# Performance work log

Hardware: AMD Instinct MI355X
Metric: run time of the kernel (lower is better)

Reference implementation:

```python
import jax, jax.numpy as jnp
import numpy as np

N_ATOMS, N_EDGES, FEAT, N_RBF, N_CONV = 20000, 320000, 128, 20, 3
CUTOFF = 5.0
ATOM_FEA, H_FEA, N_OUT, VOCAB = 64, 128, 5, 100


def _dense(x, W, b):
    return x @ W + b


def _painn_forward(xyz, embed, W1, b1, W2, b2, Wd, bd, U, V, Ws1, bs1, Ws2, bs2,
                   Wr1, br1, Wr2, br2, Wf1, bf1, Wf2, bf2, Wf3, bf3, z, nbrs):
    act = jax.nn.silu
    i_idx, j_idx = nbrs[:, 0], nbrs[:, 1]          # receiver i, sender j
    r_ij = xyz[j_idx] - xyz[i_idx]                 # [E,3]
    d = jnp.sqrt(jnp.sum(r_ij ** 2, -1) + 1e-12)   # [E]
    unit = r_ij / d[:, None]
    n = jnp.arange(1, N_RBF + 1, dtype=xyz.dtype)
    rbf = jnp.sin(n[None, :] * jnp.pi * d[:, None] / CUTOFF) / d[:, None]   # [E,n_rbf]
    f_cut = 0.5 * (jnp.cos(jnp.pi * d / CUTOFF) + 1.0) * (d < CUTOFF)       # cosine envelope

    s = embed[z]                                   # [N,F]
    v = jnp.zeros((s.shape[0], FEAT, 3), s.dtype)  # [N,F,3]

    for l in range(N_CONV):
        # ---- message block ----
        phi = _dense(act(_dense(s, W1[l], b1[l])), W2[l], b2[l])        # [N,3F]
        w_s = _dense(rbf, Wd[l], bd[l]) * f_cut[:, None]                # [E,3F]
        inv = (phi[j_idx] * w_s).reshape(-1, 3, FEAT)                   # [E,3,F]
        dv_ij = unit[:, None, :] * inv[:, 2, :, None] + inv[:, 0, :, None] * v[j_idx]  # [E,F,3]
        s = s + jax.ops.segment_sum(inv[:, 1, :], i_idx, num_segments=N_ATOMS)
        v = v + jax.ops.segment_sum(dv_ij, i_idx, num_segments=N_ATOMS)
        # ---- update block ----
        u_v = jnp.einsum('nfd,fg->ngd', v, U[l])                        # [N,F,3]
        v_v = jnp.einsum('nfd,fg->ngd', v, V[l])
        v_norm = jnp.sqrt(jnp.sum(v_v ** 2, -1) + 1e-12)                # [N,F]
        split = _dense(act(_dense(jnp.concatenate([s, v_norm], -1), Ws1[l], bs1[l])), Ws2[l], bs2[l])
        a_vv = split[:, :FEAT]
        a_sv = split[:, FEAT:2 * FEAT]
        a_ss = split[:, 2 * FEAT:]
        v = v + u_v * a_vv[:, :, None]
        s = s + jnp.sum(u_v * v_v, -1) * a_sv + a_ss

    # ---- readout (per-atom features) + fully connected head ----
    atom_fea = _dense(act(_dense(s, Wr1, br1)), Wr2, br2)               # [N,atom_fea]
    h = act(_dense(atom_fea, Wf1, bf1))
    h = act(_dense(h, Wf2, bf2))
    return _dense(h, Wf3, bf3)                                          # [N,n_outputs]


def setup_inputs() -> dict:
    key = jax.random.key(0)
    ks = jax.random.split(key, 20)
    sc = 0.08  # ~1/sqrt(feat_dim) to keep activations stable
    def rn(k, shape, s=sc):
        return jax.random.normal(k, shape, dtype=jnp.float32) * s
    return {
        'xyz': jax.random.uniform(ks[0], (N_ATOMS, 3), dtype=jnp.float32) * 4.0,
        'z': jax.random.randint(ks[1], (N_ATOMS,), 0, VOCAB),
        'nbrs': jax.random.randint(ks[2], (N_EDGES, 2), 0, N_ATOMS),
        'embed': rn(ks[3], (VOCAB, FEAT), 1.0),
        'W1': rn(ks[4], (N_CONV, FEAT, FEAT)), 'b1': jnp.zeros((N_CONV, FEAT)),
        'W2': rn(ks[5], (N_CONV, FEAT, 3 * FEAT)), 'b2': jnp.zeros((N_CONV, 3 * FEAT)),
        'Wd': rn(ks[6], (N_CONV, N_RBF, 3 * FEAT)), 'bd': jnp.zeros((N_CONV, 3 * FEAT)),
        'U': rn(ks[7], (N_CONV, FEAT, FEAT)),
        'V': rn(ks[8], (N_CONV, FEAT, FEAT)),
        'Ws1': rn(ks[9], (N_CONV, 2 * FEAT, FEAT)), 'bs1': jnp.zeros((N_CONV, FEAT)),
        'Ws2': rn(ks[10], (N_CONV, FEAT, 3 * FEAT)), 'bs2': jnp.zeros((N_CONV, 3 * FEAT)),
        'Wr1': rn(ks[11], (FEAT, FEAT)), 'br1': jnp.zeros((FEAT,)),
        'Wr2': rn(ks[12], (FEAT, ATOM_FEA)), 'br2': jnp.zeros((ATOM_FEA,)),
        'Wf1': rn(ks[13], (ATOM_FEA, H_FEA)), 'bf1': jnp.zeros((H_FEA,)),
        'Wf2': rn(ks[14], (H_FEA, H_FEA)), 'bf2': jnp.zeros((H_FEA,)),
        'Wf3': rn(ks[15], (H_FEA, N_OUT)), 'bf3': jnp.zeros((N_OUT,)),
    }


def reference(xyz, z, nbrs, embed, W1, b1, W2, b2, Wd, bd, U, V, Ws1, bs1, Ws2, bs2,
              Wr1, br1, Wr2, br2, Wf1, bf1, Wf2, bf2, Wf3, bf3):
    return _painn_forward(xyz, embed, W1, b1, W2, b2, Wd, bd, U, V, Ws1, bs1, Ws2, bs2,
                          Wr1, br1, Wr2, br2, Wf1, bf1, Wf2, bf2, Wf3, bf3, z, nbrs)
```

## Files before the change

kernel.cpp:

```cpp
#include <hip/hip_runtime.h>
#include <hip/hip_bf16.h>
#include <math.h>

#define N_ATOMS 20000
#define N_EDGES 320000
#define FEAT 128
#define N_RBF 20
#define N_CONV 3
#define N_OUT_ 5
#define PI_F 3.14159265358979f
#define M20P 20032
#define M60P 60032

typedef unsigned short ushort;
typedef __bf16 bf16x8 __attribute__((ext_vector_type(8)));
typedef float f32x4 __attribute__((ext_vector_type(4)));

__device__ __forceinline__ float b2f(ushort u){ return __uint_as_float(((unsigned)u) << 16); }
__device__ __forceinline__ ushort f2b(float x){
    unsigned u = __float_as_uint(x);
    return (ushort)((u + 0x7FFFu + ((u >> 16) & 1u)) >> 16);
}

constexpr size_t rnd64(size_t x){ return (x + 63) & ~size_t(63); }
constexpr size_t F_XYZ  = 64;
constexpr size_t F_EMB  = rnd64(F_XYZ + 60000);
constexpr size_t F_B1   = rnd64(F_EMB + 12800);
constexpr size_t F_B2   = rnd64(F_B1  + 3*128);
constexpr size_t F_WD   = rnd64(F_B2  + 3*384);
constexpr size_t F_BD   = rnd64(F_WD  + 3*20*384);
constexpr size_t F_BS1  = rnd64(F_BD  + 3*384);
constexpr size_t F_BS2  = rnd64(F_BS1 + 3*128);
constexpr size_t F_BR1  = rnd64(F_BS2 + 3*384);
constexpr size_t F_BR2  = rnd64(F_BR1 + 128);
constexpr size_t F_BF1  = rnd64(F_BR2 + 64);
constexpr size_t F_BF2  = rnd64(F_BF1 + 128);
constexpr size_t F_BF3  = rnd64(F_BF2 + 128);
constexpr size_t F_FC   = rnd64(F_BF3 + 8);
constexpr size_t F_UNIT = rnd64(F_FC   + N_EDGES);
constexpr size_t F_G    = rnd64(F_UNIT + 3*N_EDGES);
constexpr size_t F_CNT  = rnd64(F_G    + (size_t)N_EDGES*N_RBF);
constexpr size_t F_ROW  = rnd64(F_CNT  + N_ATOMS);
constexpr size_t F_CUR  = rnd64(F_ROW  + N_ATOMS + 1);
constexpr size_t F_EID  = rnd64(F_CUR  + N_ATOMS);
constexpr size_t F_S    = rnd64(F_EID  + N_EDGES);
constexpr size_t F_V    = rnd64(F_S    + (size_t)N_ATOMS*FEAT);
constexpr size_t F_PHI  = rnd64(F_V    + (size_t)60000*FEAT);
constexpr size_t F_VV   = rnd64(F_PHI  + (size_t)N_ATOMS*384);
constexpr size_t F_SPL  = rnd64(F_VV   + (size_t)60000*FEAT);
constexpr size_t F_OUT  = rnd64(F_SPL  + (size_t)N_ATOMS*384);
constexpr size_t H_SHI  = rnd64(F_OUT  + N_ATOMS*N_OUT_);
constexpr size_t H_SLO  = rnd64(H_SHI  + (size_t)M20P*128/2);
constexpr size_t H_VHI  = rnd64(H_SLO  + (size_t)M20P*128/2);
constexpr size_t H_VLO  = rnd64(H_VHI  + (size_t)M60P*128/2);
constexpr size_t H_HAHI = rnd64(H_VLO  + (size_t)M60P*128/2);
constexpr size_t H_HALO = rnd64(H_HAHI + (size_t)M20P*128/2);
constexpr size_t H_HBHI = rnd64(H_HALO + (size_t)M20P*128/2);
constexpr size_t H_HBLO = rnd64(H_HBHI + (size_t)M20P*128/2);
constexpr size_t H_AFHI = rnd64(H_HBLO + (size_t)M20P*128/2);
constexpr size_t H_AFLO = rnd64(H_AFHI + (size_t)M20P*64/2);
constexpr size_t H_WT   = rnd64(H_AFLO + (size_t)M20P*64/2);
constexpr size_t O_W1T=0, O_W2T=49152, O_UT=196608, O_VT=245760, O_WS1T=294912,
                 O_WS2T=393216, O_WR1T=540672, O_WR2T=557056, O_WF1T=565248,
                 O_WF2T=573440, O_WF3T=589824, O_WTOT=598016;

__global__ void k_detect(const unsigned int* __restrict__ bits, int* flag){
    __shared__ int cnt;
    if (threadIdx.x == 0) cnt = 0;
    __syncthreads();
    unsigned int lo = bits[threadIdx.x] & 0xFFFFu;
    if (lo >= 0x3000u && lo <= 0x4100u) atomicAdd(&cnt, 1);
    __syncthreads();
    if (threadIdx.x == 0) *flag = (cnt >= 48) ? 1 : 0;
}

struct P13 { const void* p[13]; };
__global__ void k_cvt_all(P13 sp, float* __restrict__ ws, const int* __restrict__ flag){
    constexpr int   NSEG = 13;
    constexpr int    SZ[NSEG] = {60000,12800,384,1152,23040,1152,384,1152,128,64,128,128,5};
    constexpr size_t DO_[NSEG]= {F_XYZ,F_EMB,F_B1,F_B2,F_WD,F_BD,F_BS1,F_BS2,F_BR1,F_BR2,F_BF1,F_BF2,F_BF3};
    int t = blockIdx.x * blockDim.x + threadIdx.x;
    int bf = *flag;
    #pragma unroll
    for (int s = 0; s < NSEG; s++){
        if (t < SZ[s]){
            float v = bf ? b2f(((const ushort*)sp.p[s])[t]) : ((const float*)sp.p[s])[t];
            ws[DO_[s] + t] = v;
            return;
        }
        t -= SZ[s];
    }
}

struct P11 { const void* p[11]; };
__global__ void k_wt_all(P11 sp, ushort* __restrict__ wb, const int* __restrict__ flag){
    constexpr int NSEG = 23;
    constexpr int SRC[NSEG]  = {0,1,2,3,4,5, 0,1,2,3,4,5, 0,1,2,3,4,5, 6,7,8,9,10};
    constexpr int SOFF[NSEG] = {0,0,0,0,0,0, 16384,49152,16384,16384,32768,49152,
                                32768,98304,32768,32768,65536,98304, 0,0,0,0,0};
    constexpr size_t DOFF[NSEG]={O_W1T,O_W2T,O_UT,O_VT,O_WS1T,O_WS2T,
                                 O_W1T+16384,O_W2T+49152,O_UT+16384,O_VT+16384,O_WS1T+32768,O_WS2T+49152,
                                 O_W1T+32768,O_W2T+98304,O_UT+32768,O_VT+32768,O_WS1T+65536,O_WS2T+98304,
                                 O_WR1T,O_WR2T,O_WF1T,O_WF2T,O_WF3T};
    constexpr int KK[NSEG]   = {128,128,128,128,256,128, 128,128,128,128,256,128,
                                128,128,128,128,256,128, 128,128,64,128,128};
    constexpr int NN[NSEG]   = {128,384,128,128,128,384, 128,384,128,128,128,384,
                                128,384,128,128,128,384, 128,64,128,128,5};
    constexpr int NP[NSEG]   = {128,384,128,128,128,384, 128,384,128,128,128,384,
                                128,384,128,128,128,384, 128,64,128,128,64};
    int t = blockIdx.x * blockDim.x + threadIdx.x;
    int bf = *flag;
    #pragma unroll
    for (int s = 0; s < NSEG; s++){
        int tot = NP[s] * KK[s];
        if (t < tot){
            int n = t / KK[s], k = t & (KK[s] - 1);
            ushort hi = 0, lo = 0;
            if (n < NN[s]){
                int si = SOFF[s] + k * NN[s] + n;
                float w = bf ? b2f(((const ushort*)sp.p[SRC[s]])[si])
                             : ((const float*)sp.p[SRC[s]])[si];
                hi = f2b(w); lo = f2b(w - b2f(hi));
            }
            wb[DOFF[s] + t] = hi;
            wb[O_WTOT + DOFF[s] + t] = lo;
            return;
        }
        t -= tot;
    }
}
constexpr int WT_TOTAL = 598016;

__global__ void k_store_out(const float* __restrict__ src, void* __restrict__ dst, int n,
                            const int* __restrict__ flag){
    int t = blockIdx.x * blockDim.x + threadIdx.x;
    if (t >= n) return;
    float v = src[t];
    if (*flag) ((ushort*)dst)[t] = f2b(v);
    else       ((float*)dst)[t] = v;
}

__global__ void k_zero_f(float* p, int n){
    int t = blockIdx.x * blockDim.x + threadIdx.x;
    if (t < n) p[t] = 0.f;
}
__global__ void k_zero_i(int* p, int n){
    int t = blockIdx.x * blockDim.x + threadIdx.x;
    if (t < n) p[t] = 0;
}
__global__ void k_init_s(const float* __restrict__ embed, const int* __restrict__ z,
                         float* __restrict__ s, ushort* __restrict__ shi,
                         ushort* __restrict__ slo){
    int t = blockIdx.x * blockDim.x + threadIdx.x;
    if (t >= N_ATOMS * FEAT) return;
    int n = t >> 7, f = t & 127;
    float v = embed[z[n] * FEAT + f];
    s[t] = v;
    ushort h = f2b(v); shi[t] = h; slo[t] = f2b(v - b2f(h));
}

__global__ void k_geom(const float* __restrict__ xyz, const int* __restrict__ nbrs,
                       float* __restrict__ fcb, float* __restrict__ unit,
                       float* __restrict__ G){
    int e = blockIdx.x * blockDim.x + threadIdx.x;
    if (e >= N_EDGES) return;
    int i = nbrs[2*e], j = nbrs[2*e+1];
    float rx = xyz[3*j]   - xyz[3*i];
    float ry = xyz[3*j+1] - xyz[3*i+1];
    float rz = xyz[3*j+2] - xyz[3*i+2];
    float d  = sqrtf(rx*rx + ry*ry + rz*rz + 1e-12f);
    float inv = 1.0f / d;
    unit[3*e] = rx*inv; unit[3*e+1] = ry*inv; unit[3*e+2] = rz*inv;
    float b  = PI_F * d * 0.2f;
    float sb = sinf(b), cb = cosf(b);
    float fc = (d < 5.0f) ? 0.5f * (cb + 1.0f) : 0.0f;
    fcb[e] = fc;
    float scale = inv * fc, c2 = 2.0f * cb;
    float sp = 0.f, sc = sb;
    float* g = G + (size_t)e * N_RBF;
    #pragma unroll
    for (int r = 0; r < N_RBF; r++){
        g[r] = sc * scale;
        float sn = c2 * sc - sp;
        sp = sc; sc = sn;
    }
}

__global__ void k_hist(const int* __restrict__ nbrs, int* __restrict__ cnt){
    int e = blockIdx.x * blockDim.x + threadIdx.x;
    if (e < N_EDGES) atomicAdd(&cnt[nbrs[2*e]], 1);
}
__global__ void k_scan(const int* __restrict__ cnt, int* __restrict__ row, int* __restrict__ cur){
    __shared__ int ls[256];
    int t = threadIdx.x, base = t * 80;
    int s = 0;
    for (int k = 0; k < 80; k++){ int i = base + k; if (i < N_ATOMS) s += cnt[i]; }
    ls[t] = s; __syncthreads();
    for (int off = 1; off < 256; off <<= 1){
        int v = (t >= off) ? ls[t - off] : 0;
        __syncthreads();
        ls[t] += v;
        __syncthreads();
    }
    int run = ls[t] - s;
    for (int k = 0; k < 80; k++){
        int i = base + k;
        if (i < N_ATOMS){ row[i] = run; cur[i] = run; run += cnt[i]; }
    }
    if (t == 255) row[N_ATOMS] = ls[255];
}
__global__ void k_fill(const int* __restrict__ nbrs, int* __restrict__ cur, int* __restrict__ eid){
    int e = blockIdx.x * blockDim.x + threadIdx.x;
    if (e >= N_EDGES) return;
    int p = atomicAdd(&cur[nbrs[2*e]], 1);
    eid[p] = e;
}

template<int KT>
__global__ __launch_bounds__(256) void k_gemm3t(
    const ushort* __restrict__ Ahi, const ushort* __restrict__ Alo,
    const ushort* __restrict__ Bthi, const ushort* __restrict__ Btlo,
    const float* __restrict__ bias, int M, int N, int act,
    float* __restrict__ Cf, ushort* __restrict__ Chi, ushort* __restrict__ Clo)
{
    int wave = threadIdx.x >> 6, lane = threadIdx.x & 63;
    int l15 = lane & 15, quad = lane >> 4;
    int m0 = blockIdx.y * 128 + wave * 32;
    int n0 = blockIdx.x * 64;
    const ushort* aph = Ahi  + (size_t)(m0 + l15) * KT + quad * 8;
    const ushort* apl = Alo  + (size_t)(m0 + l15) * KT + quad * 8;
    const ushort* bph = Bthi + (size_t)(n0 + l15) * KT + quad * 8;
    const ushort* bpl = Btlo + (size_t)(n0 + l15) * KT + quad * 8;
    f32x4 acc[2][4];
    #pragma unroll
    for (int r = 0; r < 2; r++)
        #pragma unroll
        for (int c = 0; c < 4; c++) acc[r][c] = (f32x4){0.f, 0.f, 0.f, 0.f};
    #pragma unroll
    for (int k0 = 0; k0 < KT; k0 += 32) {
        bf16x8 ah0 = *reinterpret_cast<const bf16x8*>(aph + k0);
        bf16x8 al0 = *reinterpret_cast<const bf16x8*>(apl + k0);
        bf16x8 ah1 = *reinterpret_cast<const bf16x8*>(aph + (size_t)16 * KT + k0);
        bf16x8 al1 = *reinterpret_cast<const bf16x8*>(apl + (size_t)16 * KT + k0);
        #pragma unroll
        for (int c = 0; c < 4; c++) {
            bf16x8 bh = *reinterpret_cast<const bf16x8*>(bph + (size_t)c * 16 * KT + k0);
            bf16x8 bl = *reinterpret_cast<const bf16x8*>(bpl + (size_t)c * 16 * KT + k0);
            acc[0][c] = __builtin_amdgcn_mfma_f32_16x16x32_bf16(al0, bh, acc[0][c], 0, 0, 0);
            acc[0][c] = __builtin_amdgcn_mfma_f32_16x16x32_bf16(ah0, bl, acc[0][c], 0, 0, 0);
            acc[0][c] = __builtin_amdgcn_mfma_f32_16x16x32_bf16(ah0, bh, acc[0][c], 0, 0, 0);
            acc[1][c] = __builtin_amdgcn_mfma_f32_16x16x32_bf16(al1, bh, acc[1][c], 0, 0, 0);
            acc[1][c] = __builtin_amdgcn_mfma_f32_16x16x32_bf16(ah1, bl, acc[1][c], 0, 0, 0);
            acc[1][c] = __builtin_amdgcn_mfma_f32_16x16x32_bf16(ah1, bh, acc[1][c], 0, 0, 0);
        }
    }
    #pragma unroll
    for (int rr = 0; rr < 2; rr++) {
        int row_base = m0 + rr * 16 + quad * 4;
        #pragma unroll
        for (int c = 0; c < 4; c++) {
            int col = n0 + c * 16 + l15;
            #pragma unroll
            for (int r = 0; r < 4; r++) {
                int row = row_base + r;
                if (row < M && col < N) {
                    float v = acc[rr][c][r];
                    if (bias) v += bias[col];
                    if (act)  v = v / (1.f + expf(-v));
                    size_t idx = (size_t)row * N + col;
                    if (Cf)  Cf[idx] = v;
                    if (Chi) { ushort h = f2b(v); Chi[idx] = h; Clo[idx] = f2b(v - b2f(h)); }
                }
            }
        }
    }
}

__global__ __launch_bounds__(256) void k_gemm3_dual(
    const ushort* __restrict__ Ahi, const ushort* __restrict__ Alo,
    const ushort* __restrict__ B1hi, const ushort* __restrict__ B1lo,
    const ushort* __restrict__ B2hi, const ushort* __restrict__ B2lo,
    int M, float* __restrict__ C1, float* __restrict__ C2)
{
    constexpr int KT = 128, N = 128;
    int wave = threadIdx.x >> 6, lane = threadIdx.x & 63;
    int l15 = lane & 15, quad = lane >> 4;
    int m0 = blockIdx.y * 128 + wave * 32;
    int n0 = blockIdx.x * 64;
    const ushort* aph = Ahi  + (size_t)(m0 + l15) * KT + quad * 8;
    const ushort* apl = Alo  + (size_t)(m0 + l15) * KT + quad * 8;
    const ushort* b1h = B1hi + (size_t)(n0 + l15) * KT + quad * 8;
    const ushort* b1l = B1lo + (size_t)(n0 + l15) * KT + quad * 8;
    const ushort* b2h = B2hi + (size_t)(n0 + l15) * KT + quad * 8;
    const ushort* b2l = B2lo + (size_t)(n0 + l15) * KT + quad * 8;
    f32x4 acc1[2][4], acc2[2][4];
    #pragma unroll
    for (int r = 0; r < 2; r++)
        #pragma unroll
        for (int c = 0; c < 4; c++) {
            acc1[r][c] = (f32x4){0.f,0.f,0.f,0.f};
            acc2[r][c] = (f32x4){0.f,0.f,0.f,0.f};
        }
    #pragma unroll
    for (int k0 = 0; k0 < KT; k0 += 32) {
        bf16x8 ah0 = *reinterpret_cast<const bf16x8*>(aph + k0);
        bf16x8 al0 = *reinterpret_cast<const bf16x8*>(apl + k0);
        bf16x8 ah1 = *reinterpret_cast<const bf16x8*>(aph + (size_t)16 * KT + k0);
        bf16x8 al1 = *reinterpret_cast<const bf16x8*>(apl + (size_t)16 * KT + k0);
        #pragma unroll
        for (int c = 0; c < 4; c++) {
            bf16x8 bh = *reinterpret_cast<const bf16x8*>(b1h + (size_t)c * 16 * KT + k0);
            bf16x8 bl = *reinterpret_cast<const bf16x8*>(b1l + (size_t)c * 16 * KT + k0);
            acc1[0][c] = __builtin_amdgcn_mfma_f32_16x16x32_bf16(al0, bh, acc1[0][c], 0, 0, 0);
            acc1[0][c] = __builtin_amdgcn_mfma_f32_16x16x32_bf16(ah0, bl, acc1[0][c], 0, 0, 0);
            acc1[0][c] = __builtin_amdgcn_mfma_f32_16x16x32_bf16(ah0, bh, acc1[0][c], 0, 0, 0);
            acc1[1][c] = __builtin_amdgcn_mfma_f32_16x16x32_bf16(al1, bh, acc1[1][c], 0, 0, 0);
            acc1[1][c] = __builtin_amdgcn_mfma_f32_16x16x32_bf16(ah1, bl, acc1[1][c], 0, 0, 0);
            acc1[1][c] = __builtin_amdgcn_mfma_f32_16x16x32_bf16(ah1, bh, acc1[1][c], 0, 0, 0);
        }
        #pragma unroll
        for (int c = 0; c < 4; c++) {
            bf16x8 bh = *reinterpret_cast<const bf16x8*>(b2h + (size_t)c * 16 * KT + k0);
            bf16x8 bl = *reinterpret_cast<const bf16x8*>(b2l + (size_t)c * 16 * KT + k0);
            acc2[0][c] = __builtin_amdgcn_mfma_f32_16x16x32_bf16(al0, bh, acc2[0][c], 0, 0, 0);
            acc2[0][c] = __builtin_amdgcn_mfma_f32_16x16x32_bf16(ah0, bl, acc2[0][c], 0, 0, 0);
            acc2[0][c] = __builtin_amdgcn_mfma_f32_16x16x32_bf16(ah0, bh, acc2[0][c], 0, 0, 0);
            acc2[1][c] = __builtin_amdgcn_mfma_f32_16x16x32_bf16(al1, bh, acc2[1][c], 0, 0, 0);
            acc2[1][c] = __builtin_amdgcn_mfma_f32_16x16x32_bf16(ah1, bl, acc2[1][c], 0, 0, 0);
            acc2[1][c] = __builtin_amdgcn_mfma_f32_16x16x32_bf16(ah1, bh, acc2[1][c], 0, 0, 0);
        }
    }
    #pragma unroll
    for (int rr = 0; rr < 2; rr++) {
        int row_base = m0 + rr * 16 + quad * 4;
        #pragma unroll
        for (int c = 0; c < 4; c++) {
            int col = n0 + c * 16 + l15;
            #pragma unroll
            for (int r = 0; r < 4; r++) {
                int row = row_base + r;
                if (row < M) {
                    size_t idx = (size_t)row * N + col;
                    C1[idx] = acc1[rr][c][r];
                    C2[idx] = acc2[rr][c][r];
                }
            }
        }
    }
}

__global__ __launch_bounds__(128) void k_edge3(
    const float* __restrict__ phi, const float* __restrict__ vin,
    const float* __restrict__ unit, const float* __restrict__ fcb,
    const float* __restrict__ G,
    const int* __restrict__ nbrs, const int* __restrict__ row, const int* __restrict__ eid,
    const float* __restrict__ Wd, const float* __restrict__ bd,
    float* __restrict__ s, ushort* __restrict__ vhi, ushort* __restrict__ vlo)
{
    int i = blockIdx.x, f = threadIdx.x;
    float wdr[3 * N_RBF];
    #pragma unroll
    for (int r = 0; r < N_RBF; r++) {
        wdr[r]           = Wd[r*384 + f];
        wdr[N_RBF + r]   = Wd[r*384 + 128 + f];
        wdr[2*N_RBF + r] = Wd[r*384 + 256 + f];
    }
    float bd0 = bd[f], bd1 = bd[128 + f], bd2 = bd[256 + f];
    float sacc = 0.f, va0 = 0.f, va1 = 0.f, va2 = 0.f;
    int beg = row[i], end = row[i + 1];
    for (int idx = beg; idx < end; idx++) {
        int e = eid[idx];
        int j = nbrs[2*e + 1];
        float fc = fcb[e];
        float w0 = bd0 * fc, w1 = bd1 * fc, w2 = bd2 * fc;
        const float* g = G + (size_t)e * N_RBF;
        #pragma unroll
        for (int r = 0; r < N_RBF; r++) {
            float gr = g[r];
            w0 = fmaf(gr, wdr[r],           w0);
            w1 = fmaf(gr, wdr[N_RBF + r],   w1);
            w2 = fmaf(gr, wdr[2*N_RBF + r], w2);
        }
        size_t pj = (size_t)j * 384;
        float inv0 = phi[pj + f]       * w0;
        float inv1 = phi[pj + 128 + f] * w1;
        float inv2 = phi[pj + 256 + f] * w2;
        float ux = unit[3*e], uy = unit[3*e+1], uz = unit[3*e+2];
        size_t vj = (size_t)j * 384 + f;
        sacc += inv1;
        va0 = fmaf(inv0, vin[vj],       fmaf(ux, inv2, va0));
        va1 = fmaf(inv0, vin[vj + 128], fmaf(uy, inv2, va1));
        va2 = fmaf(inv0, vin[vj + 256], fmaf(uz, inv2, va2));
    }
    s[(size_t)i * FEAT + f] += sacc;
    size_t vi = (size_t)i * 384 + f;
    float n0 = vin[vi] + va0, n1 = vin[vi + 128] + va1, n2 = vin[vi + 256] + va2;
    ushort h;
    h = f2b(n0); vhi[vi]       = h; vlo[vi]       = f2b(n0 - b2f(h));
    h = f2b(n1); vhi[vi + 128] = h; vlo[vi + 128] = f2b(n1 - b2f(h));
    h = f2b(n2); vhi[vi + 256] = h; vlo[vi + 256] = f2b(n2 - b2f(h));
}

__global__ void k_vnorm_cat(const float* __restrict__ s, const float* __restrict__ vv,
                            ushort* __restrict__ chi, ushort* __restrict__ clo){
    int t = blockIdx.x * blockDim.x + threadIdx.x;
    if (t >= N_ATOMS * FEAT) return;
    int n = t >> 7, g = t & 127;
    size_t b = (size_t)n * 384 + g;
    float a0 = vv[b], a1 = vv[b + 128], a2 = vv[b + 256];
    float nr = sqrtf(a0*a0 + a1*a1 + a2*a2 + 1e-12f);
    float sv = s[t];
    size_t c0 = (size_t)n * 256 + g;
    ushort h;
    h = f2b(sv); chi[c0]       = h; clo[c0]       = f2b(sv - b2f(h));
    h = f2b(nr); chi[c0 + 128] = h; clo[c0 + 128] = f2b(nr - b2f(h));
}

__global__ void k_update(const float* __restrict__ uv, const float* __restrict__ vv,
                         const float* __restrict__ spl,
                         const ushort* __restrict__ vhi, const ushort* __restrict__ vlo,
                         float* __restrict__ s, float* __restrict__ v,
                         ushort* __restrict__ shi, ushort* __restrict__ slo){
    int t = blockIdx.x * blockDim.x + threadIdx.x;
    if (t >= N_ATOMS * FEAT) return;
    int n = t >> 7, g = t & 127;
    size_t sp = (size_t)n * 384 + g;
    float avv = spl[sp], asv = spl[sp + 128], ass = spl[sp + 256];
    float dot = 0.f;
    size_t b = (size_t)n * 384 + g;
    #pragma unroll
    for (int d = 0; d < 3; d++) {
        size_t idx = b + (size_t)d * 128;
        float u  = uv[idx];
        float w  = vv[idx];
        float vb = b2f(vhi[idx]) + b2f(vlo[idx]);
        dot = fmaf(u, w, dot);
        v[idx] = vb + u * avv;
    }
    float ns = s[t] + dot * asv + ass;
    s[t] = ns;
    ushort h = f2b(ns); shi[t] = h; slo[t] = f2b(ns - b2f(h));
}

struct Pair { ushort* hi; ushort* lo; };

static inline void gemm3(Pair A, Pair B, const float* bias,
                         int M, int K, int N, int Npad, int act,
                         float* Cf, Pair C, hipStream_t s){
    dim3 g(Npad / 64, (M + 127) / 128), b(256);
    switch (K) {
    case 64:  k_gemm3t<64> <<<g, b, 0, s>>>(A.hi, A.lo, B.hi, B.lo, bias, M, N, act, Cf, C.hi, C.lo); break;
    case 128: k_gemm3t<128><<<g, b, 0, s>>>(A.hi, A.lo, B.hi, B.lo, bias, M, N, act, Cf, C.hi, C.lo); break;
    case 256: k_gemm3t<256><<<g, b, 0, s>>>(A.hi, A.lo, B.hi, B.lo, bias, M, N, act, Cf, C.hi, C.lo); break;
    }
}

extern "C" void kernel_launch(void* const* d_in, const int* in_sizes, int n_in,
                              void* d_out, int out_size, void* d_ws, size_t ws_size,
                              hipStream_t stream) {
    float* ws = (float*)d_ws;
    int* flag = (int*)d_ws;
    const int* z    = (const int*)d_in[1];
    const int* nbrs = (const int*)d_in[2];

    k_detect<<<1, 64, 0, stream>>>((const unsigned int*)d_in[0], flag);

    P13 cp; {
        const int cidx[13] = {0,3,5,7,8,9,13,15,17,19,21,23,25};
        for (int i = 0; i < 13; i++) cp.p[i] = d_in[cidx[i]];
    }
    k_cvt_all<<<(100517 + 255)/256, 256, 0, stream>>>(cp, ws, flag);

    ushort* wb = (ushort*)(ws + H_WT);
    P11 wp; {
        const int widx[11] = {4,6,10,11,12,14,16,18,20,22,24};
        for (int i = 0; i < 11; i++) wp.p[i] = d_in[widx[i]];
    }
    k_wt_all<<<(WT_TOTAL + 255)/256, 256, 0, stream>>>(wp, wb, flag);

    k_geom<<<(N_EDGES+255)/256, 256, 0, stream>>>(ws + F_XYZ, nbrs, ws + F_FC, ws + F_UNIT, ws + F_G);
    int* cnt = (int*)(ws + F_CNT); int* row = (int*)(ws + F_ROW);
    int* cur = (int*)(ws + F_CUR); int* eid = (int*)(ws + F_EID);
    k_zero_i<<<(N_ATOMS+255)/256, 256, 0, stream>>>(cnt, N_ATOMS);
    k_hist<<<(N_EDGES+255)/256, 256, 0, stream>>>(nbrs, cnt);
    k_scan<<<1, 256, 0, stream>>>(cnt, row, cur);
    k_fill<<<(N_EDGES+255)/256, 256, 0, stream>>>(nbrs, cur, eid);

    float* S   = ws + F_S;
    float* V   = ws + F_V;
    float* PHI = ws + F_PHI;
    float* VV  = ws + F_VV;
    float* SPL = ws + F_SPL;
    auto WPW = [&](size_t off){ return Pair{ wb + off, wb + O_WTOT + off }; };
    Pair SHL { (ushort*)(ws + H_SHI),  (ushort*)(ws + H_SLO)  };
    Pair VHL { (ushort*)(ws + H_VHI),  (ushort*)(ws + H_VLO)  };
    Pair HA  { (ushort*)(ws + H_HAHI), (ushort*)(ws + H_HALO) };
    Pair HB  { (ushort*)(ws + H_HBHI), (ushort*)(ws + H_HBLO) };
    Pair AF  { (ushort*)(ws + H_AFHI), (ushort*)(ws + H_AFLO) };
    Pair CAT { (ushort*)(ws + F_SPL),  (ushort*)(ws + F_SPL) + (size_t)M20P*256 };
    Pair NOP { nullptr, nullptr };

    k_init_s<<<(N_ATOMS*FEAT+255)/256, 256, 0, stream>>>(ws + F_EMB, z, S, SHL.hi, SHL.lo);
    k_zero_f<<<(60000*FEAT+255)/256, 256, 0, stream>>>(V, 60000*FEAT);

    for (int l = 0; l < N_CONV; l++) {
        gemm3(SHL, WPW(O_W1T + l*16384), ws + F_B1 + l*128, N_ATOMS, 128, 128, 128, 1, nullptr, HA, stream);
        gemm3(HA,  WPW(O_W2T + l*49152), ws + F_B2 + l*384, N_ATOMS, 128, 384, 384, 0, PHI, NOP, stream);
        k_edge3<<<N_ATOMS, 128, 0, stream>>>(PHI, V, ws + F_UNIT, ws + F_FC, ws + F_G,
                                             nbrs, row, eid,
                                             ws + F_WD + (size_t)l*20*384, ws + F_BD + l*384,
                                             S, VHL.hi, VHL.lo);
        {
            dim3 g(2, (60000 + 127) / 128), b(256);
            k_gemm3_dual<<<g, b, 0, stream>>>(VHL.hi, VHL.lo,
                                              wb + O_UT + l*16384, wb + O_WTOT + O_UT + l*16384,
                                              wb + O_VT + l*16384, wb + O_WTOT + O_VT + l*16384,
                                              60000, PHI, VV);
        }
        k_vnorm_cat<<<(N_ATOMS*FEAT+255)/256, 256, 0, stream>>>(S, VV, CAT.hi, CAT.lo);
        gemm3(CAT, WPW(O_WS1T + l*32768), ws + F_BS1 + l*128, N_ATOMS, 256, 128, 128, 1, nullptr, HB, stream);
        gemm3(HB,  WPW(O_WS2T + l*49152), ws + F_BS2 + l*384, N_ATOMS, 128, 384, 384, 0, SPL, NOP, stream);
        k_update<<<(N_ATOMS*FEAT+255)/256, 256, 0, stream>>>(PHI, VV, SPL, VHL.hi, VHL.lo,
                                                             S, V, SHL.hi, SHL.lo);
    }

    gemm3(SHL, WPW(O_WR1T), ws + F_BR1, N_ATOMS, 128, 128, 128, 1, nullptr, HA, stream);
    gemm3(HA,  WPW(O_WR2T), ws + F_BR2, N_ATOMS, 128,  64,  64, 0, nullptr, AF, stream);
    gemm3(AF,  WPW(O_WF1T), ws + F_BF1, N_ATOMS,  64, 128, 128, 1, nullptr, HB, stream);
    gemm3(HB,  WPW(O_WF2T), ws + F_BF2, N_ATOMS, 128, 128, 128, 1, nullptr, HA, stream);
    gemm3(HA,  WPW(O_WF3T), ws + F_BF3, N_ATOMS, 128, N_OUT_, 64, 0, ws + F_OUT, NOP, stream);

    k_store_out<<<(N_ATOMS*N_OUT_+255)/256, 256, 0, stream>>>(ws + F_OUT, d_out, N_ATOMS*N_OUT_, flag);
}
```

Before: 1.445 ms.

## Precompute edge geometry in CSR order as packed 24-float records

Edge geometry (cutoff, unit vector, 20 RBF values) is now computed after the CSR build and stored per sorted edge position as a packed 96-byte record, together with a separate sender-index array. The edge kernel reads each edge with six contiguous float4 loads instead of chasing eid and nbrs and reading three scattered arrays. The inner loop is also unrolled by two. The aim is to cut indirect, uncoalesced loads in the edge kernel, which runs three times. It costs a slightly larger workspace and moves the geometry kernel so it reads through eid.

```diff
diff --git a/kernel.cpp b/kernel.cpp
--- a/kernel.cpp
+++ b/kernel.cpp
@@ -36,14 +36,13 @@
 constexpr size_t F_BF1  = rnd64(F_BR2 + 64);
 constexpr size_t F_BF2  = rnd64(F_BF1 + 128);
 constexpr size_t F_BF3  = rnd64(F_BF2 + 128);
-constexpr size_t F_FC   = rnd64(F_BF3 + 8);
-constexpr size_t F_UNIT = rnd64(F_FC   + N_EDGES);
-constexpr size_t F_G    = rnd64(F_UNIT + 3*N_EDGES);
-constexpr size_t F_CNT  = rnd64(F_G    + (size_t)N_EDGES*N_RBF);
+constexpr size_t F_CNT  = rnd64(F_BF3 + 8);
 constexpr size_t F_ROW  = rnd64(F_CNT  + N_ATOMS);
 constexpr size_t F_CUR  = rnd64(F_ROW  + N_ATOMS + 1);
 constexpr size_t F_EID  = rnd64(F_CUR  + N_ATOMS);
-constexpr size_t F_S    = rnd64(F_EID  + N_EDGES);
+constexpr size_t F_EJ   = rnd64(F_EID  + N_EDGES);
+constexpr size_t F_EREC = rnd64(F_EJ   + N_EDGES);
+constexpr size_t F_S    = rnd64(F_EREC + (size_t)N_EDGES*24);
 constexpr size_t F_V    = rnd64(F_S    + (size_t)N_ATOMS*FEAT);
 constexpr size_t F_PHI  = rnd64(F_V    + (size_t)60000*FEAT);
 constexpr size_t F_VV   = rnd64(F_PHI  + (size_t)N_ATOMS*384);
@@ -159,33 +158,6 @@
     ushort h = f2b(v); shi[t] = h; slo[t] = f2b(v - b2f(h));
 }
 
-__global__ void k_geom(const float* __restrict__ xyz, const int* __restrict__ nbrs,
-                       float* __restrict__ fcb, float* __restrict__ unit,
-                       float* __restrict__ G){
-    int e = blockIdx.x * blockDim.x + threadIdx.x;
-    if (e >= N_EDGES) return;
-    int i = nbrs[2*e], j = nbrs[2*e+1];
-    float rx = xyz[3*j]   - xyz[3*i];
-    float ry = xyz[3*j+1] - xyz[3*i+1];
-    float rz = xyz[3*j+2] - xyz[3*i+2];
-    float d  = sqrtf(rx*rx + ry*ry + rz*rz + 1e-12f);
-    float inv = 1.0f / d;
-    unit[3*e] = rx*inv; unit[3*e+1] = ry*inv; unit[3*e+2] = rz*inv;
-    float b  = PI_F * d * 0.2f;
-    float sb = sinf(b), cb = cosf(b);
-    float fc = (d < 5.0f) ? 0.5f * (cb + 1.0f) : 0.0f;
-    fcb[e] = fc;
-    float scale = inv * fc, c2 = 2.0f * cb;
-    float sp = 0.f, sc = sb;
-    float* g = G + (size_t)e * N_RBF;
-    #pragma unroll
-    for (int r = 0; r < N_RBF; r++){
-        g[r] = sc * scale;
-        float sn = c2 * sc - sp;
-        sp = sc; sc = sn;
-    }
-}
-
 __global__ void k_hist(const int* __restrict__ nbrs, int* __restrict__ cnt){
     int e = blockIdx.x * blockDim.x + threadIdx.x;
     if (e < N_EDGES) atomicAdd(&cnt[nbrs[2*e]], 1);
@@ -214,6 +186,34 @@
     if (e >= N_EDGES) return;
     int p = atomicAdd(&cur[nbrs[2*e]], 1);
     eid[p] = e;
+}
+
+__global__ void k_geom_csr(const float* __restrict__ xyz, const int* __restrict__ nbrs,
+                           const int* __restrict__ eid,
+                           int* __restrict__ EJ, float* __restrict__ EREC){
+    int idx = blockIdx.x * blockDim.x + threadIdx.x;
+    if (idx >= N_EDGES) return;
+    int e = eid[idx];
+    int i = nbrs[2*e], j = nbrs[2*e+1];
+    float rx = xyz[3*j]   - xyz[3*i];
+    float ry = xyz[3*j+1] - xyz[3*i+1];
+    float rz = xyz[3*j+2] - xyz[3*i+2];
+    float d  = sqrtf(rx*rx + ry*ry + rz*rz + 1e-12f);
+    float inv = 1.0f / d;
+    float b  = PI_F * d * 0.2f;
+    float sb = sinf(b), cb = cosf(b);
+    float fc = (d < 5.0f) ? 0.5f * (cb + 1.0f) : 0.0f;
+    float scale = inv * fc, c2 = 2.0f * cb;
+    EJ[idx] = j;
+    float* rec = EREC + (size_t)idx * 24;
+    rec[0] = fc; rec[1] = rx*inv; rec[2] = ry*inv; rec[3] = rz*inv;
+    float sp = 0.f, sc = sb;
+    #pragma unroll
+    for (int r = 0; r < N_RBF; r++){
+        rec[4 + r] = sc * scale;
+        float sn = c2 * sc - sp;
+        sp = sc; sc = sn;
+    }
 }
 
 template<int KT>
@@ -349,11 +349,10 @@
     }
 }
 
-__global__ __launch_bounds__(128) void k_edge3(
+__global__ __launch_bounds__(128) void k_edge4(
     const float* __restrict__ phi, const float* __restrict__ vin,
-    const float* __restrict__ unit, const float* __restrict__ fcb,
-    const float* __restrict__ G,
-    const int* __restrict__ nbrs, const int* __restrict__ row, const int* __restrict__ eid,
+    const int* __restrict__ EJ, const float* __restrict__ EREC,
+    const int* __restrict__ row,
     const float* __restrict__ Wd, const float* __restrict__ bd,
     float* __restrict__ s, ushort* __restrict__ vhi, ushort* __restrict__ vlo)
 {
@@ -368,30 +367,36 @@
     float bd0 = bd[f], bd1 = bd[128 + f], bd2 = bd[256 + f];
     float sacc = 0.f, va0 = 0.f, va1 = 0.f, va2 = 0.f;
     int beg = row[i], end = row[i + 1];
-    for (int idx = beg; idx < end; idx++) {
-        int e = eid[idx];
-        int j = nbrs[2*e + 1];
-        float fc = fcb[e];
-        float w0 = bd0 * fc, w1 = bd1 * fc, w2 = bd2 * fc;
-        const float* g = G + (size_t)e * N_RBF;
+
+    auto body = [&](int idx){
+        int j = EJ[idx];
+        const float4* rq = reinterpret_cast<const float4*>(EREC + (size_t)idx * 24);
+        float4 q0 = rq[0], q1 = rq[1], q2 = rq[2], q3 = rq[3], q4 = rq[4], q5 = rq[5];
+        float g[20] = {q1.x,q1.y,q1.z,q1.w, q2.x,q2.y,q2.z,q2.w,
+                       q3.x,q3.y,q3.z,q3.w, q4.x,q4.y,q4.z,q4.w,
+                       q5.x,q5.y,q5.z,q5.w};
+        float w0 = bd0 * q0.x, w1 = bd1 * q0.x, w2 = bd2 * q0.x;
         #pragma unroll
         for (int r = 0; r < N_RBF; r++) {
-            float gr = g[r];
-            w0 = fmaf(gr, wdr[r],           w0);
-            w1 = fmaf(gr, wdr[N_RBF + r],   w1);
-            w2 = fmaf(gr, wdr[2*N_RBF + r], w2);
+            w0 = fmaf(g[r], wdr[r],           w0);
+            w1 = fmaf(g[r], wdr[N_RBF + r],   w1);
+            w2 = fmaf(g[r], wdr[2*N_RBF + r], w2);
         }
         size_t pj = (size_t)j * 384;
         float inv0 = phi[pj + f]       * w0;
         float inv1 = phi[pj + 128 + f] * w1;
         float inv2 = phi[pj + 256 + f] * w2;
-        float ux = unit[3*e], uy = unit[3*e+1], uz = unit[3*e+2];
         size_t vj = (size_t)j * 384 + f;
         sacc += inv1;
-        va0 = fmaf(inv0, vin[vj],       fmaf(ux, inv2, va0));
-        va1 = fmaf(inv0, vin[vj + 128], fmaf(uy, inv2, va1));
-        va2 = fmaf(inv0, vin[vj + 256], fmaf(uz, inv2, va2));
-    }
+        va0 = fmaf(inv0, vin[vj],       fmaf(q0.y, inv2, va0));
+        va1 = fmaf(inv0, vin[vj + 128], fmaf(q0.z, inv2, va1));
+        va2 = fmaf(inv0, vin[vj + 256], fmaf(q0.w, inv2, va2));
+    };
+
+    int idx = beg;
+    for (; idx + 1 < end; idx += 2) { body(idx); body(idx + 1); }
+    if (idx < end) body(idx);
+
     s[(size_t)i * FEAT + f] += sacc;
     size_t vi = (size_t)i * 384 + f;
     float n0 = vin[vi] + va0, n1 = vin[vi + 128] + va1, n2 = vin[vi + 256] + va2;
@@ -478,13 +483,14 @@
     }
     k_wt_all<<<(WT_TOTAL + 255)/256, 256, 0, stream>>>(wp, wb, flag);
 
-    k_geom<<<(N_EDGES+255)/256, 256, 0, stream>>>(ws + F_XYZ, nbrs, ws + F_FC, ws + F_UNIT, ws + F_G);
     int* cnt = (int*)(ws + F_CNT); int* row = (int*)(ws + F_ROW);
     int* cur = (int*)(ws + F_CUR); int* eid = (int*)(ws + F_EID);
+    int* EJ  = (int*)(ws + F_EJ);  float* EREC = ws + F_EREC;
     k_zero_i<<<(N_ATOMS+255)/256, 256, 0, stream>>>(cnt, N_ATOMS);
     k_hist<<<(N_EDGES+255)/256, 256, 0, stream>>>(nbrs, cnt);
     k_scan<<<1, 256, 0, stream>>>(cnt, row, cur);
     k_fill<<<(N_EDGES+255)/256, 256, 0, stream>>>(nbrs, cur, eid);
+    k_geom_csr<<<(N_EDGES+255)/256, 256, 0, stream>>>(ws + F_XYZ, nbrs, eid, EJ, EREC);
 
     float* S   = ws + F_S;
     float* V   = ws + F_V;
@@ -506,8 +512,7 @@
     for (int l = 0; l < N_CONV; l++) {
         gemm3(SHL, WPW(O_W1T + l*16384), ws + F_B1 + l*128, N_ATOMS, 128, 128, 128, 1, nullptr, HA, stream);
         gemm3(HA,  WPW(O_W2T + l*49152), ws + F_B2 + l*384, N_ATOMS, 128, 384, 384, 0, PHI, NOP, stream);
-        k_edge3<<<N_ATOMS, 128, 0, stream>>>(PHI, V, ws + F_UNIT, ws + F_FC, ws + F_G,
-                                             nbrs, row, eid,
+        k_edge4<<<N_ATOMS, 128, 0, stream>>>(PHI, V, EJ, EREC, row,
                                              ws + F_WD + (size_t)l*20*384, ws + F_BD + l*384,
                                              S, VHL.hi, VHL.lo);
         {
```

Measured after the change: 1.361 ms. 5.8% less time.
